# Optimization experiments

Measured on AMD Instinct MI355X. Metric: run time of the kernel, lower is better.

## Reference

```python
import jax, jax.numpy as jnp
import numpy as np

DIM = 1024
EPS = 1e-5

def layernorm(x, g, b):
    m = jnp.mean(x, axis=-1, keepdims=True)
    v = jnp.var(x, axis=-1, keepdims=True)
    return (x - m) / jnp.sqrt(v + EPS) * g + b

def setup_inputs() -> dict:
    key = jax.random.key(0)
    ks = jax.random.split(key, 12)
    B, L, D = 4, 2048, DIM
    s = 1.0 / np.sqrt(D)
    return {
        "q": jax.random.normal(ks[0], (B, L, D), jnp.float32),
        "k": jax.random.normal(ks[1], (B, L, D), jnp.float32),
        "v": jax.random.normal(ks[2], (B, L, D), jnp.float32),
        "gq": jnp.ones((D,), jnp.float32), "bq": jnp.zeros((D,), jnp.float32),
        "gk": jnp.ones((D,), jnp.float32), "bk": jnp.zeros((D,), jnp.float32),
        "gv": jnp.ones((D,), jnp.float32), "bv": jnp.zeros((D,), jnp.float32),
        "Wq": jax.random.uniform(ks[3], (D, D), jnp.float32, -s, s),
        "Wk": jax.random.uniform(ks[4], (D, D), jnp.float32, -s, s),
        "Wv": jax.random.uniform(ks[5], (D, D), jnp.float32, -s, s),
        "Wp": jax.random.uniform(ks[6], (D, D), jnp.float32, -s, s),
        "bp": jax.random.uniform(ks[7], (D,), jnp.float32, -s, s),
    }

def reference(q, k, v, gq, bq, gk, bk, gv, bv, Wq, Wk, Wv, Wp, bp):
    scale = DIM ** -0.5
    qn = layernorm(q, gq, bq) @ Wq.T  # [B,Q,D]
    kn = layernorm(k, gk, bk) @ Wk.T  # [B,K,D]
    vn = layernorm(v, gv, bv) @ Wv.T  # [B,K,D]
    attn = jnp.einsum('bqc,bkc->bqk', qn, kn)
    attn = jax.nn.relu(attn) * scale  # ReLU on raw scores, then scale (matches in-place *=)
    attn_mask = jax.nn.softmax(attn, axis=-1)
    out = jnp.einsum('bqk,bkc->bqc', attn_mask, vn)
    out = out @ Wp.T + bp
    return (attn, out)
```

## Files before the change

### kernel.cpp

```cpp
#include <hip/hip_runtime.h>


typedef __attribute__((ext_vector_type(8))) short short8v;
typedef __attribute__((ext_vector_type(4))) float f32x4;

#define DEVI __device__ __forceinline__

DEVI float b2f(unsigned short u) {
  union { unsigned int i; float f; } x;
  x.i = ((unsigned int)u) << 16;
  return x.f;
}
DEVI unsigned short f2b(float f) {
  union { float f; unsigned int i; } x;
  x.f = f;
  unsigned int r = x.i + 0x7fffu + ((x.i >> 16) & 1u);
  return (unsigned short)(r >> 16);
}

DEVI bool sniff_bf16(const unsigned short* wq) {
  int bad = 0;
#pragma unroll
  for (int j = 0; j < 64; ++j) bad |= (fabsf(b2f(wq[j])) > 0.0625f) ? 1 : 0;
  return bad == 0;
}

DEVI void async16(const unsigned short* g, unsigned short* l) {
  __builtin_amdgcn_global_load_lds(
      (const __attribute__((address_space(1))) void*)g,
      (__attribute__((address_space(3))) void*)l, 16, 0, 0);
}

template <int N> DEVI void wait_lgkm();
template <> DEVI void wait_lgkm<0>() { asm volatile("s_waitcnt lgkmcnt(0)" ::: "memory"); }
template <> DEVI void wait_lgkm<4>() { asm volatile("s_waitcnt lgkmcnt(4)" ::: "memory"); }
template <> DEVI void wait_lgkm<8>() { asm volatile("s_waitcnt lgkmcnt(8)" ::: "memory"); }
template <int N> DEVI void wait_vm();
template <> DEVI void wait_vm<0>() { asm volatile("s_waitcnt vmcnt(0)" ::: "memory"); }
template <> DEVI void wait_vm<6>() { asm volatile("s_waitcnt vmcnt(6)" ::: "memory"); }
template <> DEVI void wait_vm<8>() { asm volatile("s_waitcnt vmcnt(8)" ::: "memory"); }
#define SB0() __builtin_amdgcn_sched_barrier(0)

DEVI void stage_q(const unsigned short* G, int ld, unsigned short* L,
                  int w, int lane, int k0) {
  int r8 = lane >> 3;
  int scol = ((lane & 7) ^ r8) * 8;
  async16(G + (size_t)(w * 8 + r8) * ld + k0 + scol, L + (w * 8) * 64);
}
DEVI void stage_half(const unsigned short* G, int ld, unsigned short* L,
                     int w, int lane, int k0) {
  stage_q(G, ld, L, w, lane, k0);
  stage_q(G + (size_t)64 * ld, ld, L + 64 * 64, w, lane, k0);
}

template <int NB>
DEVI void gemm8_core(unsigned short* sA, unsigned short* sB,
                     const unsigned short* Ab, const unsigned short* Bb,
                     int m0, int n0, int lda, int ldb, int K, int tid,
                     f32x4 (&acc)[8][2 * NB]) {
  int lane = tid & 63, w = tid >> 6;
  int wm = w >> 2, wn = w & 3;
  int l15 = lane & 15, quad = lane >> 4;
  int rxor = l15 & 7;
  int cb0 = (quad ^ rxor) * 8;
  int cb1 = ((4 + quad) ^ rxor) * 8;
  const int nst = K >> 6;
  const int ABUF = 16384;
  const int BBUF = NB * 128 * 64;
  const unsigned short* A0 = Ab + (size_t)m0 * lda;
  const unsigned short* A1 = A0 + (size_t)128 * lda;
  const unsigned short* B0 = Bb + (size_t)n0 * ldb;
  const unsigned short* B1 = B0 + (size_t)128 * ldb;

  stage_half(A0, lda, sA, w, lane, 0);
  stage_half(A1, lda, sA + 8192, w, lane, 0);
  stage_half(B0, ldb, sB, w, lane, 0);
  if constexpr (NB == 2) stage_half(B1, ldb, sB + 8192, w, lane, 0);
  if (nst > 1) {
    stage_half(A0, lda, sA + ABUF, w, lane, 64);
    stage_half(A1, lda, sA + ABUF + 8192, w, lane, 64);
    stage_half(B0, ldb, sB + BBUF, w, lane, 64);
    if constexpr (NB == 2) {
      stage_half(B1, ldb, sB + BBUF + 8192, w, lane, 64);
      wait_vm<8>();
    } else {
      wait_vm<6>();
    }
  } else {
    wait_vm<0>();
  }
  __builtin_amdgcn_s_barrier();
  SB0();

  short8v a03[4][2], a47[4][2], b01[2][2], b23[2][2];
  {
    const unsigned short* rA = sA + (wm * 128 + l15) * 64;
    const unsigned short* rB = sB + (wn * (NB * 32) + l15) * 64;
#pragma unroll
    for (int mt = 0; mt < 4; ++mt) {
      a03[mt][0] = *(const short8v*)(rA + mt * 1024 + cb0);
      a03[mt][1] = *(const short8v*)(rA + mt * 1024 + cb1);
    }
#pragma unroll
    for (int nt = 0; nt < 2; ++nt) {
      b01[nt][0] = *(const short8v*)(rB + nt * 1024 + cb0);
      b01[nt][1] = *(const short8v*)(rB + nt * 1024 + cb1);
    }
  }

  for (int t = 0; t < nst; ++t) {
    const int b = t & 1;
    const bool st = (t + 1 < nst);
    const int kn = (t + 1) << 6;
    const unsigned short* rA = sA + b * ABUF + (wm * 128 + l15) * 64;
    const unsigned short* rB = sB + b * BBUF + (wn * (NB * 32) + l15) * 64;
    const unsigned short* rAn = sA + (b ^ 1) * ABUF + (wm * 128 + l15) * 64;
    const unsigned short* rBn = sB + (b ^ 1) * BBUF + (wn * (NB * 32) + l15) * 64;

    if constexpr (NB == 2) {
      if (st) {
        stage_half(A0, lda, sA + (b ^ 1) * ABUF, w, lane, kn);
        stage_half(A1, lda, sA + (b ^ 1) * ABUF + 8192, w, lane, kn);
      }
#pragma unroll
      for (int mt = 0; mt < 4; ++mt) {
        a47[mt][0] = *(const short8v*)(rA + (4 + mt) * 1024 + cb0);
        a47[mt][1] = *(const short8v*)(rA + (4 + mt) * 1024 + cb1);
      }
      wait_lgkm<8>();
      SB0();
      __builtin_amdgcn_s_setprio(1);
#pragma unroll
      for (int mt = 0; mt < 4; ++mt)
#pragma unroll
        for (int nt = 0; nt < 2; ++nt) {
          acc[mt][nt] = __builtin_amdgcn_mfma_f32_16x16x32_bf16(a03[mt][0], b01[nt][0], acc[mt][nt], 0, 0, 0);
          acc[mt][nt] = __builtin_amdgcn_mfma_f32_16x16x32_bf16(a03[mt][1], b01[nt][1], acc[mt][nt], 0, 0, 0);
        }
      __builtin_amdgcn_s_setprio(0);

      if (st) {
        stage_half(B0, ldb, sB + (b ^ 1) * BBUF, w, lane, kn);
        stage_half(B1, ldb, sB + (b ^ 1) * BBUF + 8192, w, lane, kn);
      }
#pragma unroll
      for (int nt = 0; nt < 2; ++nt) {
        b23[nt][0] = *(const short8v*)(rB + (2 + nt) * 1024 + cb0);
        b23[nt][1] = *(const short8v*)(rB + (2 + nt) * 1024 + cb1);
      }
      wait_lgkm<4>();
      SB0();
      __builtin_amdgcn_s_setprio(1);
#pragma unroll
      for (int mt = 0; mt < 4; ++mt)
#pragma unroll
        for (int nt = 0; nt < 2; ++nt) {
          acc[4 + mt][nt] = __builtin_amdgcn_mfma_f32_16x16x32_bf16(a47[mt][0], b01[nt][0], acc[4 + mt][nt], 0, 0, 0);
          acc[4 + mt][nt] = __builtin_amdgcn_mfma_f32_16x16x32_bf16(a47[mt][1], b01[nt][1], acc[4 + mt][nt], 0, 0, 0);
        }
      __builtin_amdgcn_s_setprio(0);

      wait_lgkm<0>();
      SB0();
      __builtin_amdgcn_s_setprio(1);
#pragma unroll
      for (int mt = 0; mt < 4; ++mt)
#pragma unroll
        for (int nt = 0; nt < 2; ++nt) {
          acc[mt][2 + nt] = __builtin_amdgcn_mfma_f32_16x16x32_bf16(a03[mt][0], b23[nt][0], acc[mt][2 + nt], 0, 0, 0);
          acc[mt][2 + nt] = __builtin_amdgcn_mfma_f32_16x16x32_bf16(a03[mt][1], b23[nt][1], acc[mt][2 + nt], 0, 0, 0);
        }
      __builtin_amdgcn_s_setprio(0);

      if (st) {
        wait_vm<0>();
        __builtin_amdgcn_s_barrier();
        SB0();
#pragma unroll
        for (int mt = 0; mt < 4; ++mt) {
          a03[mt][0] = *(const short8v*)(rAn + mt * 1024 + cb0);
          a03[mt][1] = *(const short8v*)(rAn + mt * 1024 + cb1);
        }
#pragma unroll
        for (int nt = 0; nt < 2; ++nt) {
          b01[nt][0] = *(const short8v*)(rBn + nt * 1024 + cb0);
          b01[nt][1] = *(const short8v*)(rBn + nt * 1024 + cb1);
        }
      }
      __builtin_amdgcn_s_setprio(1);
#pragma unroll
      for (int mt = 0; mt < 4; ++mt)
#pragma unroll
        for (int nt = 0; nt < 2; ++nt) {
          acc[4 + mt][2 + nt] = __builtin_amdgcn_mfma_f32_16x16x32_bf16(a47[mt][0], b23[nt][0], acc[4 + mt][2 + nt], 0, 0, 0);
          acc[4 + mt][2 + nt] = __builtin_amdgcn_mfma_f32_16x16x32_bf16(a47[mt][1], b23[nt][1], acc[4 + mt][2 + nt], 0, 0, 0);
        }
      __builtin_amdgcn_s_setprio(0);
    } else {
      if (st) {
        stage_half(A0, lda, sA + (b ^ 1) * ABUF, w, lane, kn);
        stage_half(A1, lda, sA + (b ^ 1) * ABUF + 8192, w, lane, kn);
        stage_half(B0, ldb, sB + (b ^ 1) * BBUF, w, lane, kn);
      }
#pragma unroll
      for (int mt = 0; mt < 4; ++mt) {
        a47[mt][0] = *(const short8v*)(rA + (4 + mt) * 1024 + cb0);
        a47[mt][1] = *(const short8v*)(rA + (4 + mt) * 1024 + cb1);
      }
      wait_lgkm<8>();
      SB0();
      __builtin_amdgcn_s_setprio(1);
#pragma unroll
      for (int mt = 0; mt < 4; ++mt)
#pragma unroll
        for (int nt = 0; nt < 2; ++nt) {
          acc[mt][nt] = __builtin_amdgcn_mfma_f32_16x16x32_bf16(a03[mt][0], b01[nt][0], acc[mt][nt], 0, 0, 0);
          acc[mt][nt] = __builtin_amdgcn_mfma_f32_16x16x32_bf16(a03[mt][1], b01[nt][1], acc[mt][nt], 0, 0, 0);
        }
      __builtin_amdgcn_s_setprio(0);

      wait_lgkm<0>();
      SB0();
      if (st) {
        wait_vm<0>();
        __builtin_amdgcn_s_barrier();
        SB0();
#pragma unroll
        for (int mt = 0; mt < 4; ++mt) {
          a03[mt][0] = *(const short8v*)(rAn + mt * 1024 + cb0);
          a03[mt][1] = *(const short8v*)(rAn + mt * 1024 + cb1);
        }
      }
      __builtin_amdgcn_s_setprio(1);
#pragma unroll
      for (int mt = 0; mt < 4; ++mt)
#pragma unroll
        for (int nt = 0; nt < 2; ++nt) {
          acc[4 + mt][nt] = __builtin_amdgcn_mfma_f32_16x16x32_bf16(a47[mt][0], b01[nt][0], acc[4 + mt][nt], 0, 0, 0);
          acc[4 + mt][nt] = __builtin_amdgcn_mfma_f32_16x16x32_bf16(a47[mt][1], b01[nt][1], acc[4 + mt][nt], 0, 0, 0);
        }
      __builtin_amdgcn_s_setprio(0);
      if (st) {
#pragma unroll
        for (int nt = 0; nt < 2; ++nt) {
          b01[nt][0] = *(const short8v*)(rBn + nt * 1024 + cb0);
          b01[nt][1] = *(const short8v*)(rBn + nt * 1024 + cb1);
        }
      }
    }
  }
}

DEVI int xcd_swz(int f, int nb) { return (f & 7) * (nb >> 3) + (f >> 3); }

struct PrepArgs {
  const void* q; const void* k; const void* v;
  const void* g[3]; const void* b[3];
  const void* W[4];
};

__global__ __launch_bounds__(256) void k_prep(PrepArgs pa,
    unsigned short* __restrict__ Wb, unsigned short* __restrict__ XN) {
  bool isbf = sniff_bf16((const unsigned short*)pa.W[0]);
  int bid = blockIdx.x, tid = threadIdx.x;
  if (bid < 2048) {
    int s = bid >> 9;
    size_t inner = ((size_t)(bid & 511)) * 2048 + (size_t)tid * 8;
    unsigned short* dst = Wb + (size_t)s * 1048576 + inner;
    if (isbf) {
      *(uint4*)dst = *(const uint4*)((const unsigned short*)pa.W[s] + inner);
    } else {
      const float* f = (const float*)pa.W[s] + inner;
      float4 a = *(const float4*)f;
      float4 b = *(const float4*)(f + 4);
      ushort4 o0 = { f2b(a.x), f2b(a.y), f2b(a.z), f2b(a.w) };
      ushort4 o1 = { f2b(b.x), f2b(b.y), f2b(b.z), f2b(b.w) };
      *(ushort4*)dst = o0;
      *(ushort4*)(dst + 4) = o1;
    }
  } else {
    int rb = bid - 2048;
    int wv = tid >> 6, lane = tid & 63;
    int row = rb * 4 + wv;
    int t = row >> 13;
    size_t r = (size_t)(row & 8191);
    const void* src = (t == 0) ? pa.q : (t == 1) ? pa.k : pa.v;
    float x[16];
    if (isbf) {
      const unsigned short* s = (const unsigned short*)src + r * 1024;
#pragma unroll
      for (int j = 0; j < 2; ++j) {
        uint4 pk = *(const uint4*)(s + j * 512 + lane * 8);
        const unsigned short* ps = (const unsigned short*)&pk;
#pragma unroll
        for (int e = 0; e < 8; ++e) x[j * 8 + e] = b2f(ps[e]);
      }
    } else {
      const float* s = (const float*)src + r * 1024;
#pragma unroll
      for (int j = 0; j < 4; ++j) {
        float4 pk = *(const float4*)(s + j * 256 + lane * 4);
        x[j * 4 + 0] = pk.x; x[j * 4 + 1] = pk.y;
        x[j * 4 + 2] = pk.z; x[j * 4 + 3] = pk.w;
      }
    }
    float s1 = 0.f, s2 = 0.f;
#pragma unroll
    for (int e = 0; e < 16; ++e) { s1 += x[e]; s2 += x[e] * x[e]; }
    for (int off = 32; off > 0; off >>= 1) {
      s1 += __shfl_xor(s1, off);
      s2 += __shfl_xor(s2, off);
    }
    float m  = s1 * (1.0f / 1024.0f);
    float m2 = s2 * (1.0f / 1024.0f);
    float rstd = rsqrtf(m2 - m * m + 1e-5f);
    unsigned short* dst = XN + (size_t)row * 1024;
    if (isbf) {
      const unsigned short* gp = (const unsigned short*)pa.g[t];
      const unsigned short* bp = (const unsigned short*)pa.b[t];
#pragma unroll
      for (int j = 0; j < 2; ++j) {
        uint4 gk = *(const uint4*)(gp + j * 512 + lane * 8);
        uint4 bk = *(const uint4*)(bp + j * 512 + lane * 8);
        const unsigned short* gs = (const unsigned short*)&gk;
        const unsigned short* bs = (const unsigned short*)&bk;
        uint4 out;
        unsigned short* os = (unsigned short*)&out;
#pragma unroll
        for (int e = 0; e < 8; ++e)
          os[e] = f2b((x[j * 8 + e] - m) * rstd * b2f(gs[e]) + b2f(bs[e]));
        *(uint4*)(dst + j * 512 + lane * 8) = out;
      }
    } else {
      const float* gp = (const float*)pa.g[t];
      const float* bp = (const float*)pa.b[t];
#pragma unroll
      for (int j = 0; j < 4; ++j) {
        float4 gk = *(const float4*)(gp + j * 256 + lane * 4);
        float4 bk = *(const float4*)(bp + j * 256 + lane * 4);
        ushort4 o;
        o.x = f2b((x[j * 4 + 0] - m) * rstd * gk.x + bk.x);
        o.y = f2b((x[j * 4 + 1] - m) * rstd * gk.y + bk.y);
        o.z = f2b((x[j * 4 + 2] - m) * rstd * gk.z + bk.z);
        o.w = f2b((x[j * 4 + 3] - m) * rstd * gk.w + bk.w);
        *(ushort4*)(dst + j * 256 + lane * 4) = o;
      }
    }
  }
}

__global__ __launch_bounds__(512, 2) void k_megaproj(
    const unsigned short* __restrict__ XN, const unsigned short* __restrict__ Wb,
    unsigned short* __restrict__ QN, unsigned short* __restrict__ VNT) {
  __shared__ __align__(16) unsigned short sA[2 * 256 * 64];
  __shared__ __align__(16) unsigned short sB[2 * 256 * 64];
  int x = blockIdx.x, tid = threadIdx.x;
  int lane = tid & 63, w = tid >> 6;
  int wm = w >> 2, wn = w & 3;
  int l15 = lane & 15, quad = lane >> 4;

  if (x < 256) {
    int i = xcd_swz(x, 256);
    int t = i >> 7, j = i & 127;
    int m0 = (j >> 2) * 256, n0 = (j & 3) * 256;
    f32x4 acc[8][4];
#pragma unroll
    for (int a = 0; a < 8; ++a)
#pragma unroll
      for (int c = 0; c < 4; ++c) acc[a][c] = (f32x4){0.f, 0.f, 0.f, 0.f};
    gemm8_core<2>(sA, sB, XN + (size_t)t * 8388608, Wb + (size_t)t * 1048576,
                  m0, n0, 1024, 1024, 1024, tid, acc);
    unsigned short* C = QN + (size_t)t * 8388608;
#pragma unroll
    for (int mt = 0; mt < 8; ++mt) {
      int mb = m0 + wm * 128 + mt * 16 + quad * 4;
#pragma unroll
      for (int nt = 0; nt < 4; ++nt) {
        int n = n0 + wn * 64 + nt * 16 + l15;
        f32x4 vc = acc[mt][nt];
#pragma unroll
        for (int r2 = 0; r2 < 4; ++r2) C[(size_t)(mb + r2) * 1024 + n] = f2b(vc[r2]);
      }
    }
  } else {
    int i = xcd_swz(x - 256, 256);
    int z = i >> 6, j = i & 63;
    int m0 = (j >> 4) * 256, n0 = (j & 15) * 128;
    f32x4 acc[8][2];
#pragma unroll
    for (int a = 0; a < 8; ++a)
#pragma unroll
      for (int c = 0; c < 2; ++c) acc[a][c] = (f32x4){0.f, 0.f, 0.f, 0.f};
    gemm8_core<1>(sA, sB, Wb + 2 * 1048576, XN + 2 * 8388608 + (size_t)z * 2097152,
                  m0, n0, 1024, 1024, 1024, tid, acc);
    unsigned short* C = VNT + (size_t)z * 2097152;
#pragma unroll
    for (int mt = 0; mt < 8; ++mt) {
      int mb = m0 + wm * 128 + mt * 16 + quad * 4;
#pragma unroll
      for (int nt = 0; nt < 2; ++nt) {
        int n = n0 + wn * 32 + nt * 16 + l15;
        f32x4 vc = acc[mt][nt];
#pragma unroll
        for (int r2 = 0; r2 < 4; ++r2) C[(size_t)(mb + r2) * 2048 + n] = f2b(vc[r2]);
      }
    }
  }
}

template <int EPI, int NB>
__global__ __launch_bounds__(512, 2) void k_gemm(
    const unsigned short* __restrict__ A, const unsigned short* __restrict__ B,
    void* __restrict__ Cv, long long coff,
    int K, int lda, int ldb, int ldc,
    long long sAb, long long sBb, long long sCb,
    float scale, const void* __restrict__ bias,
    const unsigned short* __restrict__ wq_sniff) {
  __shared__ __align__(16) unsigned short sA[2 * 256 * 64];
  __shared__ __align__(16) unsigned short sB[2 * NB * 128 * 64];
  int tid = threadIdx.x;
  int lane = tid & 63, w = tid >> 6;
  int wm = w >> 2, wn = w & 3;
  int l15 = lane & 15, quad = lane >> 4;

  int gx = gridDim.x, gy = gridDim.y;
  int nb = gx * gy * (int)gridDim.z;
  int f = (int)blockIdx.x + gx * ((int)blockIdx.y + gy * (int)blockIdx.z);
  f = xcd_swz(f, nb);
  int bx = f % gx;
  int rem = f / gx;
  int by = rem % gy;
  int bz = rem / gy;

  int m0 = by * 256, n0 = bx * (NB * 128);
  f32x4 acc[8][2 * NB];
#pragma unroll
  for (int i = 0; i < 8; ++i)
#pragma unroll
    for (int j = 0; j < 2 * NB; ++j) acc[i][j] = (f32x4){0.f, 0.f, 0.f, 0.f};

  gemm8_core<NB>(sA, sB, A + (long long)bz * sAb, B + (long long)bz * sBb,
                 m0, n0, lda, ldb, K, tid, acc);

  long long cbase = coff + (long long)bz * sCb;
  bool isbf = (EPI != 0) ? sniff_bf16(wq_sniff) : true;
#pragma unroll
  for (int mt = 0; mt < 8; ++mt) {
    int mb = m0 + wm * 128 + mt * 16 + quad * 4;
#pragma unroll
    for (int nt = 0; nt < 2 * NB; ++nt) {
      int n = n0 + wn * (NB * 32) + nt * 16 + l15;
      f32x4 vc = acc[mt][nt];
      if (EPI == 0) {
        unsigned short* C = (unsigned short*)Cv + cbase;
#pragma unroll
        for (int r2 = 0; r2 < 4; ++r2) C[(size_t)(mb + r2) * ldc + n] = f2b(vc[r2]);
      } else if (EPI == 1) {
        if (isbf) {
          unsigned short* C = (unsigned short*)Cv + cbase;
#pragma unroll
          for (int r2 = 0; r2 < 4; ++r2)
            C[(size_t)(mb + r2) * ldc + n] = f2b(fmaxf(vc[r2], 0.f) * scale);
        } else {
          float* C = (float*)Cv + cbase;
#pragma unroll
          for (int r2 = 0; r2 < 4; ++r2)
            C[(size_t)(mb + r2) * ldc + n] = fmaxf(vc[r2], 0.f) * scale;
        }
      } else {
        float bv2 = isbf ? b2f(((const unsigned short*)bias)[n])
                         : ((const float*)bias)[n];
        if (isbf) {
          unsigned short* C = (unsigned short*)Cv + cbase;
#pragma unroll
          for (int r2 = 0; r2 < 4; ++r2) C[(size_t)(mb + r2) * ldc + n] = f2b(vc[r2] + bv2);
        } else {
          float* C = (float*)Cv + cbase;
#pragma unroll
          for (int r2 = 0; r2 < 4; ++r2) C[(size_t)(mb + r2) * ldc + n] = vc[r2] + bv2;
        }
      }
    }
  }
}

__global__ __launch_bounds__(256) void k_softmax(const void* __restrict__ S,
    unsigned short* __restrict__ P, const unsigned short* __restrict__ wq_sniff) {
  bool isbf = sniff_bf16(wq_sniff);
  size_t row = blockIdx.x;
  int tid = threadIdx.x;
  float v[8];
  if (isbf) {
    const unsigned short* s = (const unsigned short*)S + row * 2048 + (size_t)tid * 8;
    ushort4 a = *(const ushort4*)s;
    ushort4 b = *(const ushort4*)(s + 4);
    v[0] = b2f(a.x); v[1] = b2f(a.y); v[2] = b2f(a.z); v[3] = b2f(a.w);
    v[4] = b2f(b.x); v[5] = b2f(b.y); v[6] = b2f(b.z); v[7] = b2f(b.w);
  } else {
    const float* s = (const float*)S + row * 2048 + (size_t)tid * 8;
    float4 a = *(const float4*)s;
    float4 b = *(const float4*)(s + 4);
    v[0] = a.x; v[1] = a.y; v[2] = a.z; v[3] = a.w;
    v[4] = b.x; v[5] = b.y; v[6] = b.z; v[7] = b.w;
  }
  float mx = v[0];
#pragma unroll
  for (int j = 1; j < 8; ++j) mx = fmaxf(mx, v[j]);
  for (int off = 32; off > 0; off >>= 1) mx = fmaxf(mx, __shfl_down(mx, off));
  __shared__ float sh[8];
  if ((tid & 63) == 0) sh[tid >> 6] = mx;
  __syncthreads();
  mx = fmaxf(fmaxf(sh[0], sh[1]), fmaxf(sh[2], sh[3]));
  float sum = 0.f;
#pragma unroll
  for (int j = 0; j < 8; ++j) { v[j] = __expf(v[j] - mx); sum += v[j]; }
  for (int off = 32; off > 0; off >>= 1) sum += __shfl_down(sum, off);
  if ((tid & 63) == 0) sh[4 + (tid >> 6)] = sum;
  __syncthreads();
  float inv = 1.0f / (sh[4] + sh[5] + sh[6] + sh[7]);
  ushort4 o0 = { f2b(v[0] * inv), f2b(v[1] * inv), f2b(v[2] * inv), f2b(v[3] * inv) };
  ushort4 o1 = { f2b(v[4] * inv), f2b(v[5] * inv), f2b(v[6] * inv), f2b(v[7] * inv) };
  unsigned short* p = P + row * 2048 + (size_t)tid * 8;
  *(ushort4*)p = o0;
  *(ushort4*)(p + 4) = o1;
}

static const size_t MB_ = 1024 * 1024;
static const size_t OFF_W   = 0;
static const size_t OFF_XN  = 8 * MB_ + 128 * 1024;
static const size_t OFF_QN  = OFF_XN + 48 * MB_;
static const size_t OFF_VNT = OFF_QN + 32 * MB_;
static const size_t OFF_P   = OFF_XN;
static const size_t OFF_O1  = OFF_XN + 32 * MB_;

extern "C" void kernel_launch(void* const* d_in, const int* in_sizes, int n_in,
                              void* d_out, int out_size, void* d_ws, size_t ws_size,
                              hipStream_t stream) {
  (void)in_sizes; (void)n_in; (void)out_size; (void)ws_size;
  char* ws = (char*)d_ws;
  unsigned short* Wb  = (unsigned short*)(ws + OFF_W);
  unsigned short* XN  = (unsigned short*)(ws + OFF_XN);
  unsigned short* QN  = (unsigned short*)(ws + OFF_QN);
  unsigned short* VNT = (unsigned short*)(ws + OFF_VNT);
  unsigned short* P   = (unsigned short*)(ws + OFF_P);
  unsigned short* O1  = (unsigned short*)(ws + OFF_O1);
  const unsigned short* WqS = (const unsigned short*)d_in[9];

  PrepArgs pa;
  pa.q = d_in[0]; pa.k = d_in[1]; pa.v = d_in[2];
  pa.g[0] = d_in[3]; pa.b[0] = d_in[4];
  pa.g[1] = d_in[5]; pa.b[1] = d_in[6];
  pa.g[2] = d_in[7]; pa.b[2] = d_in[8];
  pa.W[0] = d_in[9]; pa.W[1] = d_in[10]; pa.W[2] = d_in[11]; pa.W[3] = d_in[12];

  k_prep<<<8192, 256, 0, stream>>>(pa, Wb, XN);

  k_megaproj<<<512, 512, 0, stream>>>(XN, Wb, QN, VNT);

  k_gemm<1, 2><<<dim3(8, 8, 4), 512, 0, stream>>>(
      QN, QN + 8388608, d_out,
      0,
      1024, 1024, 1024, 2048,
      2097152LL, 2097152LL, 4194304LL,
      0.03125f, nullptr, WqS);

  k_softmax<<<8192, 256, 0, stream>>>(d_out, P, WqS);

  k_gemm<0, 1><<<dim3(8, 8, 4), 512, 0, stream>>>(
      P, VNT, O1,
      0,
      2048, 2048, 2048, 1024,
      4194304LL, 2097152LL, 2097152LL,
      0.f, nullptr, WqS);

  k_gemm<3, 1><<<dim3(8, 32, 1), 512, 0, stream>>>(
      O1, Wb + 3 * 1048576, d_out,
      16777216,
      1024, 1024, 1024, 1024,
      0LL, 0LL, 0LL,
      0.f, d_in[13], WqS);
}
```

Measured before the change: 385.0 us.

## Deepen GEMM global-to-LDS prefetch to two tiles ahead

```diff
diff --git a/kernel.cpp b/kernel.cpp
--- a/kernel.cpp
+++ b/kernel.cpp
@@ -72,20 +72,19 @@
   const unsigned short* B0 = Bb + (size_t)n0 * ldb;
   const unsigned short* B1 = B0 + (size_t)128 * ldb;
 
-  stage_half(A0, lda, sA, w, lane, 0);
-  stage_half(A1, lda, sA + 8192, w, lane, 0);
-  stage_half(B0, ldb, sB, w, lane, 0);
-  if constexpr (NB == 2) stage_half(B1, ldb, sB + 8192, w, lane, 0);
+  auto stage_tile = [&](int buf, int k0) {
+    stage_half(A0, lda, sA + buf * ABUF, w, lane, k0);
+    stage_half(A1, lda, sA + buf * ABUF + 8192, w, lane, k0);
+    stage_half(B0, ldb, sB + buf * BBUF, w, lane, k0);
+    if constexpr (NB == 2)
+      stage_half(B1, ldb, sB + buf * BBUF + 8192, w, lane, k0);
+  };
+
+  stage_tile(0, 0);
   if (nst > 1) {
-    stage_half(A0, lda, sA + ABUF, w, lane, 64);
-    stage_half(A1, lda, sA + ABUF + 8192, w, lane, 64);
-    stage_half(B0, ldb, sB + BBUF, w, lane, 64);
-    if constexpr (NB == 2) {
-      stage_half(B1, ldb, sB + BBUF + 8192, w, lane, 64);
-      wait_vm<8>();
-    } else {
-      wait_vm<6>();
-    }
+    stage_tile(1, 64);
+    if constexpr (NB == 2) wait_vm<8>();
+    else                   wait_vm<6>();
   } else {
     wait_vm<0>();
   }
@@ -110,18 +109,13 @@
 
   for (int t = 0; t < nst; ++t) {
     const int b = t & 1;
-    const bool st = (t + 1 < nst);
-    const int kn = (t + 1) << 6;
+    const bool st1 = (t + 1 < nst), st2 = (t + 2 < nst);
     const unsigned short* rA = sA + b * ABUF + (wm * 128 + l15) * 64;
     const unsigned short* rB = sB + b * BBUF + (wn * (NB * 32) + l15) * 64;
     const unsigned short* rAn = sA + (b ^ 1) * ABUF + (wm * 128 + l15) * 64;
     const unsigned short* rBn = sB + (b ^ 1) * BBUF + (wn * (NB * 32) + l15) * 64;
 
     if constexpr (NB == 2) {
-      if (st) {
-        stage_half(A0, lda, sA + (b ^ 1) * ABUF, w, lane, kn);
-        stage_half(A1, lda, sA + (b ^ 1) * ABUF + 8192, w, lane, kn);
-      }
 #pragma unroll
       for (int mt = 0; mt < 4; ++mt) {
         a47[mt][0] = *(const short8v*)(rA + (4 + mt) * 1024 + cb0);
@@ -139,10 +133,6 @@
         }
       __builtin_amdgcn_s_setprio(0);
 
-      if (st) {
-        stage_half(B0, ldb, sB + (b ^ 1) * BBUF, w, lane, kn);
-        stage_half(B1, ldb, sB + (b ^ 1) * BBUF + 8192, w, lane, kn);
-      }
 #pragma unroll
       for (int nt = 0; nt < 2; ++nt) {
         b23[nt][0] = *(const short8v*)(rB + (2 + nt) * 1024 + cb0);
@@ -172,9 +162,15 @@
         }
       __builtin_amdgcn_s_setprio(0);
 
-      if (st) {
-        wait_vm<0>();
+      if (st1) {
         __builtin_amdgcn_s_barrier();
+        SB0();
+        if (st2) {
+          stage_tile(b, (t + 2) << 6);
+          wait_vm<8>();
+        } else {
+          wait_vm<0>();
+        }
         SB0();
 #pragma unroll
         for (int mt = 0; mt < 4; ++mt) {
@@ -197,11 +193,6 @@
         }
       __builtin_amdgcn_s_setprio(0);
     } else {
-      if (st) {
-        stage_half(A0, lda, sA + (b ^ 1) * ABUF, w, lane, kn);
-        stage_half(A1, lda, sA + (b ^ 1) * ABUF + 8192, w, lane, kn);
-        stage_half(B0, ldb, sB + (b ^ 1) * BBUF, w, lane, kn);
-      }
 #pragma unroll
       for (int mt = 0; mt < 4; ++mt) {
         a47[mt][0] = *(const short8v*)(rA + (4 + mt) * 1024 + cb0);
@@ -221,9 +212,15 @@
 
       wait_lgkm<0>();
       SB0();
-      if (st) {
-        wait_vm<0>();
+      if (st1) {
         __builtin_amdgcn_s_barrier();
+        SB0();
+        if (st2) {
+          stage_tile(b, (t + 2) << 6);
+          wait_vm<6>();
+        } else {
+          wait_vm<0>();
+        }
         SB0();
 #pragma unroll
         for (int mt = 0; mt < 4; ++mt) {
@@ -240,7 +237,7 @@
           acc[4 + mt][nt] = __builtin_amdgcn_mfma_f32_16x16x32_bf16(a47[mt][1], b01[nt][1], acc[4 + mt][nt], 0, 0, 0);
         }
       __builtin_amdgcn_s_setprio(0);
-      if (st) {
+      if (st1) {
 #pragma unroll
         for (int nt = 0; nt < 2; ++nt) {
           b01[nt][0] = *(const short8v*)(rBn + nt * 1024 + cb0);
```

New measurement: 396.7 us. 3.0% more time.
